# Kernel optimization log

Hardware: AMD Instinct MI355X
Metric: run time of the kernel (lower is better)

## Reference

```python
import jax, jax.numpy as jnp
import numpy as np

DIM = 768
H = 12  # num_heads -> head width W = 64 (required by internal reshapes)


def setup_inputs() -> dict:
    key = jax.random.key(0)
    ks = jax.random.split(key, 16)
    B, S = 1, 128  # V = Q = A = 128 tokens
    d = {
        "v": jax.random.normal(ks[0], (B, S, DIM), jnp.float32),
        "q": jax.random.normal(ks[1], (B, S, DIM), jnp.float32),
        "a": jax.random.normal(ks[2], (B, S, DIM), jnp.float32),
        "v_mask": jnp.ones((B, S), jnp.bool_),  # unused by the module, kept for signature parity
        "q_mask": jnp.ones((B, S), jnp.bool_),
        "a_mask": jnp.ones((B, S), jnp.bool_),
    }
    scale = 0.02
    names = ["Wv", "Wq", "Wa", "Wvo", "Wqo", "Wao"]
    for i, n in enumerate(names):
        d[n] = jax.random.normal(ks[3 + i], (DIM, DIM), jnp.float32) * scale
        d["b" + n[1:].lower()] = jnp.zeros((DIM,), jnp.float32)
    return d


def _heads(x):
    # (B, S, D) -> (B, H, S, W)
    B, S, D = x.shape
    return x.reshape(B, S, H, D // H).transpose(0, 2, 1, 3)


def reference(v, q, a, v_mask, q_mask, a_mask,
              Wv, bv, Wq, bq, Wa, ba, Wvo, bvo, Wqo, bqo, Wao, bao):
    B, Sv, D = v.shape
    Sq, Sa = q.shape[1], a.shape[1]
    W = D // H
    nv, nq, na = Sv // 8, Sq // 8, Sa // 8

    # first projections (masks are unused in the original forward)
    vp = v @ Wv + bv
    qp = q @ Wq + bq
    ap = a @ Wa + ba
    # output projections are applied to the ALREADY-projected tensors (as in source)
    vo = vp @ Wvo + bvo
    qo = qp @ Wqo + bqo
    ao = ap @ Wao + bao

    vh, qh, ah = _heads(vp), _heads(qp), _heads(ap)          # (B,H,S,W)
    voh, qoh, aoh = _heads(vo), _heads(qo), _heads(ao)

    # trilinear scores: (B,H,V,Q,A)
    att = jnp.einsum('bhvw,bhqw,bhaw->bhvqa', vh, qh, ah) / jnp.sqrt(jnp.asarray(W, vh.dtype))
    K = nv * nq * na
    # faithful to source: view(-1, H, nv*nq*na) then softmax over last axis, view back
    att = jax.nn.softmax(att.reshape(-1, H, K), axis=-1)
    att = att.reshape(-1, H, nv, nq, na)  # dropout p=0 -> identity
    B2 = att.shape[0]

    # source uses att.size(2) (= nv) for ALL three reshapes (requires V=Q=A)
    vor = voh.reshape(B2, H, nv, -1)
    qor = qoh.reshape(B2, H, nv, -1)
    aor = aoh.reshape(B2, H, nv, -1)

    v_out = jnp.einsum('bhvqa,bhvw->bvhw', att, vor).reshape(-1, DIM)
    q_out = jnp.einsum('bhvqa,bhqw->bqhw', att, qor).reshape(-1, DIM)
    a_out = jnp.einsum('bhvqa,bhaw->bahw', att, aor).reshape(-1, DIM)
    return (v_out, q_out, a_out)
```

## Files before the change

kernel.cpp:

```cpp
#include <hip/hip_runtime.h>


#define DIM   768
#define SEQ   128
#define NH    12
#define HW    64
#define PROJ_ELEMS (SEQ * DIM)
#define QOUT_OFF   98304
#define AOUT_OFF   196608

typedef short bf16x8 __attribute__((ext_vector_type(8)));
typedef short bf16x4 __attribute__((ext_vector_type(4)));
typedef float f32x4  __attribute__((ext_vector_type(4)));

__device__ __forceinline__ short f2bf(float f) {
    unsigned u = __float_as_uint(f);
    u = (u + 0x7FFFu + ((u >> 16) & 1u)) >> 16;
    return (short)u;
}

__global__ __launch_bounds__(256) void proj_mfma_kernel(
    const float* __restrict__ A0, const float* __restrict__ A1, const float* __restrict__ A2,
    const float* __restrict__ W0, const float* __restrict__ W1, const float* __restrict__ W2,
    const float* __restrict__ b0, const float* __restrict__ b1, const float* __restrict__ b2,
    float* __restrict__ C0, float* __restrict__ C1, float* __restrict__ C2)
{
    const int mat = blockIdx.y;
    const float* __restrict__ A  = (mat == 0) ? A0 : (mat == 1) ? A1 : A2;
    const float* __restrict__ Wm = (mat == 0) ? W0 : (mat == 1) ? W1 : W2;
    const float* __restrict__ bb = (mat == 0) ? b0 : (mat == 1) ? b1 : b2;
    float* __restrict__ C        = (mat == 0) ? C0 : (mat == 1) ? C1 : C2;
    const int n0 = blockIdx.x * 32;

    __shared__ short Bl[2][32][136];

    const int t    = threadIdx.x;
    const int w    = t >> 6;
    const int lane = t & 63;
    const int fm   = lane & 15;
    const int fk   = (lane >> 4) << 3;

    const int kp = (t >> 3) << 2;
    const int np = (t & 7) << 2;

    f32x4 acc[2][2];
    #pragma unroll
    for (int mt = 0; mt < 2; ++mt)
        #pragma unroll
        for (int nt = 0; nt < 2; ++nt)
            acc[mt][nt] = (f32x4){0.f, 0.f, 0.f, 0.f};

    f32x4 wr[4];
    #pragma unroll
    for (int rr = 0; rr < 4; ++rr)
        wr[rr] = *(const f32x4*)&Wm[(kp + rr) * DIM + n0 + np];

    for (int s = 0; s < 6; ++s) {
        f32x4 wn[4];
        if (s < 5) {
            #pragma unroll
            for (int rr = 0; rr < 4; ++rr)
                wn[rr] = *(const f32x4*)&Wm[((s + 1) * 128 + kp + rr) * DIM + n0 + np];
        }
        f32x4 alo[2][4], ahi[2][4];
        #pragma unroll
        for (int mt = 0; mt < 2; ++mt)
            #pragma unroll
            for (int ks = 0; ks < 4; ++ks) {
                const float* pa = &A[(32 * w + 16 * mt + fm) * DIM + s * 128 + 32 * ks + fk];
                alo[mt][ks] = *(const f32x4*)pa;
                ahi[mt][ks] = *(const f32x4*)(pa + 4);
            }
        const int buf = s & 1;
        #pragma unroll
        for (int c = 0; c < 4; ++c) {
            bf16x4 pk;
            pk[0] = f2bf(wr[0][c]); pk[1] = f2bf(wr[1][c]);
            pk[2] = f2bf(wr[2][c]); pk[3] = f2bf(wr[3][c]);
            *(bf16x4*)&Bl[buf][np + c][kp] = pk;
        }
        __syncthreads();
        #pragma unroll
        for (int ks = 0; ks < 4; ++ks) {
            bf16x8 bfr0 = *(const bf16x8*)&Bl[buf][fm     ][32 * ks + fk];
            bf16x8 bfr1 = *(const bf16x8*)&Bl[buf][16 + fm][32 * ks + fk];
            #pragma unroll
            for (int mt = 0; mt < 2; ++mt) {
                bf16x8 afr;
                afr[0] = f2bf(alo[mt][ks][0]); afr[1] = f2bf(alo[mt][ks][1]);
                afr[2] = f2bf(alo[mt][ks][2]); afr[3] = f2bf(alo[mt][ks][3]);
                afr[4] = f2bf(ahi[mt][ks][0]); afr[5] = f2bf(ahi[mt][ks][1]);
                afr[6] = f2bf(ahi[mt][ks][2]); afr[7] = f2bf(ahi[mt][ks][3]);
                acc[mt][0] = __builtin_amdgcn_mfma_f32_16x16x32_bf16(afr, bfr0, acc[mt][0], 0, 0, 0);
                acc[mt][1] = __builtin_amdgcn_mfma_f32_16x16x32_bf16(afr, bfr1, acc[mt][1], 0, 0, 0);
            }
        }
        #pragma unroll
        for (int rr = 0; rr < 4; ++rr) wr[rr] = wn[rr];
    }

    const int quad4 = (lane >> 4) << 2;
    #pragma unroll
    for (int mt = 0; mt < 2; ++mt) {
        const int row0 = 32 * w + 16 * mt + quad4;
        #pragma unroll
        for (int nt = 0; nt < 2; ++nt) {
            const int col  = n0 + 16 * nt + fm;
            const float bi = bb[col];
            #pragma unroll
            for (int rr = 0; rr < 4; ++rr)
                C[(row0 + rr) * DIM + col] = acc[mt][nt][rr] + bi;
        }
    }
}

__device__ __forceinline__ float fetch_o(const float* __restrict__ p, int idx) {
    return p[((idx >> 6) & 127) * DIM + (idx >> 13) * HW + (idx & 63)];
}

__global__ __launch_bounds__(256) void fused_attn_kernel(
    const float* __restrict__ vp, const float* __restrict__ qp, const float* __restrict__ ap,
    const float* __restrict__ vo, const float* __restrict__ qo, const float* __restrict__ ao,
    float* __restrict__ out)
{
    const int vtok = blockIdx.x;
    const int h    = blockIdx.y;

    __shared__ short vqL[128][72];
    __shared__ short ahL[128][72];

    const int t    = threadIdx.x;
    const int w    = t >> 6;
    const int lane = t & 63;
    const int fm   = lane & 15;
    const int fk   = (lane >> 4) << 3;

    {
        const int r     = t >> 1;
        const int hh    = (t & 1) << 5;
        const int gcol  = h * HW + hh;
        bf16x8 vqpk[4], ahpk[4];
        #pragma unroll
        for (int u = 0; u < 8; ++u) {
            f32x4 q4 = *(const f32x4*)&qp[r    * DIM + gcol + 4 * u];
            f32x4 v4 = *(const f32x4*)&vp[vtok * DIM + gcol + 4 * u];
            f32x4 a4 = *(const f32x4*)&ap[r    * DIM + gcol + 4 * u];
            #pragma unroll
            for (int c = 0; c < 4; ++c) {
                const int idx = 4 * u + c;
                vqpk[idx >> 3][idx & 7] = f2bf(q4[c] * v4[c]);
                ahpk[idx >> 3][idx & 7] = f2bf(a4[c]);
            }
        }
        #pragma unroll
        for (int u2 = 0; u2 < 4; ++u2) {
            *(bf16x8*)&vqL[r][hh + 8 * u2] = vqpk[u2];
            *(bf16x8*)&ahL[r][hh + 8 * u2] = ahpk[u2];
        }
    }
    __syncthreads();

    f32x4 acc[2][8];
    #pragma unroll
    for (int qt = 0; qt < 2; ++qt)
        #pragma unroll
        for (int at = 0; at < 8; ++at)
            acc[qt][at] = (f32x4){0.f, 0.f, 0.f, 0.f};

    const int q0 = 32 * w;
    #pragma unroll
    for (int ks = 0; ks < 2; ++ks) {
        bf16x8 afr0 = *(const bf16x8*)&vqL[q0 + fm     ][32 * ks + fk];
        bf16x8 afr1 = *(const bf16x8*)&vqL[q0 + 16 + fm][32 * ks + fk];
        #pragma unroll
        for (int at = 0; at < 8; ++at) {
            bf16x8 bfr = *(const bf16x8*)&ahL[16 * at + fm][32 * ks + fk];
            acc[0][at] = __builtin_amdgcn_mfma_f32_16x16x32_bf16(afr0, bfr, acc[0][at], 0, 0, 0);
            acc[1][at] = __builtin_amdgcn_mfma_f32_16x16x32_bf16(afr1, bfr, acc[1][at], 0, 0, 0);
        }
    }

    float mx = -1e30f;
    #pragma unroll
    for (int qt = 0; qt < 2; ++qt)
        #pragma unroll
        for (int at = 0; at < 8; ++at)
            #pragma unroll
            for (int rr = 0; rr < 4; ++rr) {
                acc[qt][at][rr] *= 0.125f;
                mx = fmaxf(mx, acc[qt][at][rr]);
            }
    #pragma unroll
    for (int d = 1; d < 64; d <<= 1) mx = fmaxf(mx, __shfl_xor(mx, d, 64));

    float sv[2][2] = {{0.f, 0.f}, {0.f, 0.f}};
    float sq[2][8];
    #pragma unroll
    for (int i = 0; i < 2; ++i)
        #pragma unroll
        for (int j = 0; j < 8; ++j) sq[i][j] = 0.f;
    float sa = 0.f;
    #pragma unroll
    for (int qt = 0; qt < 2; ++qt)
        #pragma unroll
        for (int at = 0; at < 8; ++at)
            #pragma unroll
            for (int rr = 0; rr < 4; ++rr) {
                const float e = __expf(acc[qt][at][rr] - mx);
                sv[qt][rr >> 1] += e;
                sq[rr & 1][at]  += e;
                sa += e;
            }
    float tot = sv[0][0] + sv[0][1] + sv[1][0] + sv[1][1];

    #pragma unroll
    for (int d = 1; d < 64; d <<= 1) tot += __shfl_xor(tot, d, 64);
    #pragma unroll
    for (int dd = 0; dd < 4; ++dd) {
        const int d = 1 << dd;
        #pragma unroll
        for (int qt = 0; qt < 2; ++qt)
            #pragma unroll
            for (int rh = 0; rh < 2; ++rh)
                sv[qt][rh] += __shfl_xor(sv[qt][rh], d, 64);
    }
    #pragma unroll
    for (int dd = 0; dd < 6; ++dd) {
        const int d = 1 << dd;
        #pragma unroll
        for (int i = 0; i < 2; ++i)
            #pragma unroll
            for (int j = 0; j < 8; ++j)
                sq[i][j] += __shfl_xor(sq[i][j], d, 64);
    }
    sa += __shfl_xor(sa, 16, 64);
    sa += __shfl_xor(sa, 32, 64);

    const int g  = h * 512 + vtok * 4 + w;
    const int b2 = g / 12;
    const int h2 = g - b2 * 12;
    const float invZ = 1.0f / tot;

    if (fm == 0) {
        const int quad = lane >> 4;
        #pragma unroll
        for (int qt = 0; qt < 2; ++qt)
            #pragma unroll
            for (int rh = 0; rh < 2; ++rh) {
                const int bin = qt * 8 + quad * 2 + rh;
                out[(b2 * 16 + bin) * 12 + h2] =
                    sv[qt][rh] * invZ * fetch_o(vo, g * 16 + bin);
            }
    }
    if (lane == 0) {
        #pragma unroll
        for (int i = 0; i < 2; ++i)
            #pragma unroll
            for (int j = 0; j < 8; ++j) {
                const int bin = i * 8 + j;
                out[QOUT_OFF + (b2 * 16 + bin) * 12 + h2] =
                    sq[i][j] * invZ * fetch_o(qo, g * 16 + bin);
            }
    }
    if (lane < 16) {
        out[AOUT_OFF + (b2 * 16 + lane) * 12 + h2] =
            sa * invZ * fetch_o(ao, g * 16 + lane);
    }
}

extern "C" void kernel_launch(void* const* d_in, const int* in_sizes, int n_in,
                              void* d_out, int out_size, void* d_ws, size_t ws_size,
                              hipStream_t stream)
{
    const float* v   = (const float*)d_in[0];
    const float* q   = (const float*)d_in[1];
    const float* a   = (const float*)d_in[2];
    const float* Wv  = (const float*)d_in[6];
    const float* bv  = (const float*)d_in[7];
    const float* Wq  = (const float*)d_in[8];
    const float* bq  = (const float*)d_in[9];
    const float* Wa  = (const float*)d_in[10];
    const float* ba  = (const float*)d_in[11];
    const float* Wvo = (const float*)d_in[12];
    const float* bvo = (const float*)d_in[13];
    const float* Wqo = (const float*)d_in[14];
    const float* bqo = (const float*)d_in[15];
    const float* Wao = (const float*)d_in[16];
    const float* bao = (const float*)d_in[17];

    float* out = (float*)d_out;
    float* ws  = (float*)d_ws;
    float* vp = ws + 0 * PROJ_ELEMS;
    float* qp = ws + 1 * PROJ_ELEMS;
    float* ap = ws + 2 * PROJ_ELEMS;
    float* vo = ws + 3 * PROJ_ELEMS;
    float* qo = ws + 4 * PROJ_ELEMS;
    float* ao = ws + 5 * PROJ_ELEMS;

    proj_mfma_kernel<<<dim3(24, 3), 256, 0, stream>>>(
        v, q, a, Wv, Wq, Wa, bv, bq, ba, vp, qp, ap);
    proj_mfma_kernel<<<dim3(24, 3), 256, 0, stream>>>(
        vp, qp, ap, Wvo, Wqo, Wao, bvo, bqo, bao, vo, qo, ao);
    fused_attn_kernel<<<dim3(SEQ, NH), 256, 0, stream>>>(
        vp, qp, ap, vo, qo, ao, out);
}
```

Before: 150.5 us.

## Switch to fp16 pre-transposed weights, drop softmax max pass, transpose-reduce shuffles

A new prep kernel converts and transposes all six weight matrices to fp16, and converts the three inputs to fp16, every call. The projection GEMM then loads MFMA fragments straight from global memory with no LDS staging, and the first projection writes fp16 outputs. The attention kernel reads the fp16 projections directly (ah goes straight from global, no LDS copy). It skips the softmax max subtraction, assuming scores are small enough not to overflow, and replaces the per-bin shuffle reductions with transpose-style reductions. This trades an extra kernel launch and fp16 range/precision risk for less conversion work, fewer shuffles and less LDS traffic.

```diff
diff --git a/kernel.cpp b/kernel.cpp
--- a/kernel.cpp
+++ b/kernel.cpp
@@ -6,97 +6,104 @@
 #define NH    12
 #define HW    64
 #define PROJ_ELEMS (SEQ * DIM)
+#define WELEMS     (DIM * DIM)
 #define QOUT_OFF   98304
 #define AOUT_OFF   196608
 
-typedef short bf16x8 __attribute__((ext_vector_type(8)));
-typedef short bf16x4 __attribute__((ext_vector_type(4)));
-typedef float f32x4  __attribute__((ext_vector_type(4)));
-
-__device__ __forceinline__ short f2bf(float f) {
-    unsigned u = __float_as_uint(f);
-    u = (u + 0x7FFFu + ((u >> 16) & 1u)) >> 16;
-    return (short)u;
-}
-
-__global__ __launch_bounds__(256) void proj_mfma_kernel(
-    const float* __restrict__ A0, const float* __restrict__ A1, const float* __restrict__ A2,
+typedef _Float16 f16x8 __attribute__((ext_vector_type(8)));
+typedef float    f32x4 __attribute__((ext_vector_type(4)));
+
+__global__ __launch_bounds__(256) void prep_kernel(
+    const float* __restrict__ v, const float* __restrict__ q, const float* __restrict__ a,
     const float* __restrict__ W0, const float* __restrict__ W1, const float* __restrict__ W2,
+    const float* __restrict__ W3, const float* __restrict__ W4, const float* __restrict__ W5,
+    _Float16* __restrict__ Wt,
+    _Float16* __restrict__ vI, _Float16* __restrict__ qI, _Float16* __restrict__ aI)
+{
+    const int z = blockIdx.z;
+    const int t = threadIdx.x;
+    if (z < 6) {
+        const float* W = (z == 0) ? W0 : (z == 1) ? W1 : (z == 2) ? W2
+                       : (z == 3) ? W3 : (z == 4) ? W4 : W5;
+        _Float16* WtM = Wt + z * WELEMS;
+        __shared__ _Float16 T[64][72];
+        const int k0 = blockIdx.x * 64;
+        const int n0 = blockIdx.y * 64;
+        const int c4 = (t & 15) * 4;
+        #pragma unroll
+        for (int p = 0; p < 4; ++p) {
+            const int r = (t >> 4) + 16 * p;
+            f32x4 wv = *(const f32x4*)&W[(k0 + r) * DIM + n0 + c4];
+            T[c4 + 0][r] = (_Float16)wv[0];
+            T[c4 + 1][r] = (_Float16)wv[1];
+            T[c4 + 2][r] = (_Float16)wv[2];
+            T[c4 + 3][r] = (_Float16)wv[3];
+        }
+        __syncthreads();
+        const int c2 = (t & 7) * 8;
+        #pragma unroll
+        for (int p = 0; p < 2; ++p) {
+            const int r = (t >> 3) + 32 * p;
+            *(f16x8*)&WtM[(n0 + r) * DIM + k0 + c2] = *(const f16x8*)&T[r][c2];
+        }
+    } else {
+        const int bid = blockIdx.x + 12 * blockIdx.y;
+        const int mat = bid / 48;
+        const int off = (bid - mat * 48) * 2048 + t * 8;
+        const float* src = (mat == 0) ? v : (mat == 1) ? q : a;
+        _Float16* dst    = (mat == 0) ? vI : (mat == 1) ? qI : aI;
+        f32x4 lo = *(const f32x4*)&src[off];
+        f32x4 hi = *(const f32x4*)&src[off + 4];
+        f16x8 o;
+        o[0] = (_Float16)lo[0]; o[1] = (_Float16)lo[1];
+        o[2] = (_Float16)lo[2]; o[3] = (_Float16)lo[3];
+        o[4] = (_Float16)hi[0]; o[5] = (_Float16)hi[1];
+        o[6] = (_Float16)hi[2]; o[7] = (_Float16)hi[3];
+        *(f16x8*)&dst[off] = o;
+    }
+}
+
+__global__ __launch_bounds__(256) void proj_kernel(
+    const _Float16* __restrict__ A0, const _Float16* __restrict__ A1, const _Float16* __restrict__ A2,
+    const _Float16* __restrict__ T0, const _Float16* __restrict__ T1, const _Float16* __restrict__ T2,
     const float* __restrict__ b0, const float* __restrict__ b1, const float* __restrict__ b2,
-    float* __restrict__ C0, float* __restrict__ C1, float* __restrict__ C2)
+    void* __restrict__ C0, void* __restrict__ C1, void* __restrict__ C2,
+    int out_f16)
 {
     const int mat = blockIdx.y;
-    const float* __restrict__ A  = (mat == 0) ? A0 : (mat == 1) ? A1 : A2;
-    const float* __restrict__ Wm = (mat == 0) ? W0 : (mat == 1) ? W1 : W2;
-    const float* __restrict__ bb = (mat == 0) ? b0 : (mat == 1) ? b1 : b2;
-    float* __restrict__ C        = (mat == 0) ? C0 : (mat == 1) ? C1 : C2;
-    const int n0 = blockIdx.x * 32;
-
-    __shared__ short Bl[2][32][136];
-
+    const _Float16* __restrict__ A = (mat == 0) ? A0 : (mat == 1) ? A1 : A2;
+    const _Float16* __restrict__ T = (mat == 0) ? T0 : (mat == 1) ? T1 : T2;
+    const float* __restrict__ bb   = (mat == 0) ? b0 : (mat == 1) ? b1 : b2;
+    void* __restrict__ C           = (mat == 0) ? C0 : (mat == 1) ? C1 : C2;
+
+    const int n0   = blockIdx.x * 32;
     const int t    = threadIdx.x;
     const int w    = t >> 6;
     const int lane = t & 63;
     const int fm   = lane & 15;
     const int fk   = (lane >> 4) << 3;
 
-    const int kp = (t >> 3) << 2;
-    const int np = (t & 7) << 2;
+    const _Float16* pa0 = A + (32 * w + fm) * DIM + fk;
+    const _Float16* pa1 = pa0 + 16 * DIM;
+    const _Float16* pb0 = T + (n0 + fm) * DIM + fk;
+    const _Float16* pb1 = pb0 + 16 * DIM;
 
     f32x4 acc[2][2];
     #pragma unroll
-    for (int mt = 0; mt < 2; ++mt)
-        #pragma unroll
-        for (int nt = 0; nt < 2; ++nt)
-            acc[mt][nt] = (f32x4){0.f, 0.f, 0.f, 0.f};
-
-    f32x4 wr[4];
-    #pragma unroll
-    for (int rr = 0; rr < 4; ++rr)
-        wr[rr] = *(const f32x4*)&Wm[(kp + rr) * DIM + n0 + np];
-
-    for (int s = 0; s < 6; ++s) {
-        f32x4 wn[4];
-        if (s < 5) {
-            #pragma unroll
-            for (int rr = 0; rr < 4; ++rr)
-                wn[rr] = *(const f32x4*)&Wm[((s + 1) * 128 + kp + rr) * DIM + n0 + np];
-        }
-        f32x4 alo[2][4], ahi[2][4];
-        #pragma unroll
-        for (int mt = 0; mt < 2; ++mt)
-            #pragma unroll
-            for (int ks = 0; ks < 4; ++ks) {
-                const float* pa = &A[(32 * w + 16 * mt + fm) * DIM + s * 128 + 32 * ks + fk];
-                alo[mt][ks] = *(const f32x4*)pa;
-                ahi[mt][ks] = *(const f32x4*)(pa + 4);
-            }
-        const int buf = s & 1;
-        #pragma unroll
-        for (int c = 0; c < 4; ++c) {
-            bf16x4 pk;
-            pk[0] = f2bf(wr[0][c]); pk[1] = f2bf(wr[1][c]);
-            pk[2] = f2bf(wr[2][c]); pk[3] = f2bf(wr[3][c]);
-            *(bf16x4*)&Bl[buf][np + c][kp] = pk;
-        }
-        __syncthreads();
-        #pragma unroll
-        for (int ks = 0; ks < 4; ++ks) {
-            bf16x8 bfr0 = *(const bf16x8*)&Bl[buf][fm     ][32 * ks + fk];
-            bf16x8 bfr1 = *(const bf16x8*)&Bl[buf][16 + fm][32 * ks + fk];
-            #pragma unroll
-            for (int mt = 0; mt < 2; ++mt) {
-                bf16x8 afr;
-                afr[0] = f2bf(alo[mt][ks][0]); afr[1] = f2bf(alo[mt][ks][1]);
-                afr[2] = f2bf(alo[mt][ks][2]); afr[3] = f2bf(alo[mt][ks][3]);
-                afr[4] = f2bf(ahi[mt][ks][0]); afr[5] = f2bf(ahi[mt][ks][1]);
-                afr[6] = f2bf(ahi[mt][ks][2]); afr[7] = f2bf(ahi[mt][ks][3]);
-                acc[mt][0] = __builtin_amdgcn_mfma_f32_16x16x32_bf16(afr, bfr0, acc[mt][0], 0, 0, 0);
-                acc[mt][1] = __builtin_amdgcn_mfma_f32_16x16x32_bf16(afr, bfr1, acc[mt][1], 0, 0, 0);
-            }
-        }
-        #pragma unroll
-        for (int rr = 0; rr < 4; ++rr) wr[rr] = wn[rr];
+    for (int i = 0; i < 2; ++i)
+        #pragma unroll
+        for (int j = 0; j < 2; ++j) acc[i][j] = (f32x4){0.f, 0.f, 0.f, 0.f};
+
+    #pragma unroll 4
+    for (int s = 0; s < 24; ++s) {
+        const f16x8 a0 = *(const f16x8*)(pa0 + 32 * s);
+        const f16x8 a1 = *(const f16x8*)(pa1 + 32 * s);
+        const f16x8 w0 = *(const f16x8*)(pb0 + 32 * s);
+        const f16x8 w1 = *(const f16x8*)(pb1 + 32 * s);
+        acc[0][0] = __builtin_amdgcn_mfma_f32_16x16x32_f16(a0, w0, acc[0][0], 0, 0, 0);
+        acc[0][1] = __builtin_amdgcn_mfma_f32_16x16x32_f16(a0, w1, acc[0][1], 0, 0, 0);
+        acc[1][0] = __builtin_amdgcn_mfma_f32_16x16x32_f16(a1, w0, acc[1][0], 0, 0, 0);
+        acc[1][1] = __builtin_amdgcn_mfma_f32_16x16x32_f16(a1, w1, acc[1][1], 0, 0, 0);
     }
 
     const int quad4 = (lane >> 4) << 2;
@@ -105,11 +112,14 @@
         const int row0 = 32 * w + 16 * mt + quad4;
         #pragma unroll
         for (int nt = 0; nt < 2; ++nt) {
-            const int col  = n0 + 16 * nt + fm;
+            const int col = n0 + 16 * nt + fm;
             const float bi = bb[col];
             #pragma unroll
-            for (int rr = 0; rr < 4; ++rr)
-                C[(row0 + rr) * DIM + col] = acc[mt][nt][rr] + bi;
+            for (int rr = 0; rr < 4; ++rr) {
+                const float val = acc[mt][nt][rr] + bi;
+                if (out_f16) ((_Float16*)C)[(row0 + rr) * DIM + col] = (_Float16)val;
+                else         ((float*)C)[(row0 + rr) * DIM + col]    = val;
+            }
         }
     }
 }
@@ -119,15 +129,15 @@
 }
 
 __global__ __launch_bounds__(256) void fused_attn_kernel(
-    const float* __restrict__ vp, const float* __restrict__ qp, const float* __restrict__ ap,
+    const _Float16* __restrict__ vpH, const _Float16* __restrict__ qpH,
+    const _Float16* __restrict__ apH,
     const float* __restrict__ vo, const float* __restrict__ qo, const float* __restrict__ ao,
     float* __restrict__ out)
 {
     const int vtok = blockIdx.x;
     const int h    = blockIdx.y;
 
-    __shared__ short vqL[128][72];
-    __shared__ short ahL[128][72];
+    __shared__ _Float16 vqL[128][72];
 
     const int t    = threadIdx.x;
     const int w    = t >> 6;
@@ -136,26 +146,15 @@
     const int fk   = (lane >> 4) << 3;
 
     {
-        const int r     = t >> 1;
-        const int hh    = (t & 1) << 5;
-        const int gcol  = h * HW + hh;
-        bf16x8 vqpk[4], ahpk[4];
-        #pragma unroll
-        for (int u = 0; u < 8; ++u) {
-            f32x4 q4 = *(const f32x4*)&qp[r    * DIM + gcol + 4 * u];
-            f32x4 v4 = *(const f32x4*)&vp[vtok * DIM + gcol + 4 * u];
-            f32x4 a4 = *(const f32x4*)&ap[r    * DIM + gcol + 4 * u];
-            #pragma unroll
-            for (int c = 0; c < 4; ++c) {
-                const int idx = 4 * u + c;
-                vqpk[idx >> 3][idx & 7] = f2bf(q4[c] * v4[c]);
-                ahpk[idx >> 3][idx & 7] = f2bf(a4[c]);
-            }
-        }
-        #pragma unroll
-        for (int u2 = 0; u2 < 4; ++u2) {
-            *(bf16x8*)&vqL[r][hh + 8 * u2] = vqpk[u2];
-            *(bf16x8*)&ahL[r][hh + 8 * u2] = ahpk[u2];
+        const int r  = t >> 1;
+        const int kh = (t & 1) << 5;
+        const _Float16* pq = qpH + r    * DIM + h * HW + kh;
+        const _Float16* pv = vpH + vtok * DIM + h * HW + kh;
+        #pragma unroll
+        for (int u = 0; u < 4; ++u) {
+            const f16x8 qv = *(const f16x8*)(pq + 8 * u);
+            const f16x8 vv = *(const f16x8*)(pv + 8 * u);
+            *(f16x8*)&vqL[r][kh + 8 * u] = qv * vv;
         }
     }
     __syncthreads();
@@ -170,99 +169,93 @@
     const int q0 = 32 * w;
     #pragma unroll
     for (int ks = 0; ks < 2; ++ks) {
-        bf16x8 afr0 = *(const bf16x8*)&vqL[q0 + fm     ][32 * ks + fk];
-        bf16x8 afr1 = *(const bf16x8*)&vqL[q0 + 16 + fm][32 * ks + fk];
+        const f16x8 af0 = *(const f16x8*)&vqL[q0 + fm     ][32 * ks + fk];
+        const f16x8 af1 = *(const f16x8*)&vqL[q0 + 16 + fm][32 * ks + fk];
         #pragma unroll
         for (int at = 0; at < 8; ++at) {
-            bf16x8 bfr = *(const bf16x8*)&ahL[16 * at + fm][32 * ks + fk];
-            acc[0][at] = __builtin_amdgcn_mfma_f32_16x16x32_bf16(afr0, bfr, acc[0][at], 0, 0, 0);
-            acc[1][at] = __builtin_amdgcn_mfma_f32_16x16x32_bf16(afr1, bfr, acc[1][at], 0, 0, 0);
-        }
-    }
-
-    float mx = -1e30f;
+            const f16x8 bf = *(const f16x8*)&apH[(16 * at + fm) * DIM + h * HW + 32 * ks + fk];
+            acc[0][at] = __builtin_amdgcn_mfma_f32_16x16x32_f16(af0, bf, acc[0][at], 0, 0, 0);
+            acc[1][at] = __builtin_amdgcn_mfma_f32_16x16x32_f16(af1, bf, acc[1][at], 0, 0, 0);
+        }
+    }
+
+    float sv[2][2] = {{0.f, 0.f}, {0.f, 0.f}};
+    float sq[2][8];
+    #pragma unroll
+    for (int i = 0; i < 2; ++i)
+        #pragma unroll
+        for (int j = 0; j < 8; ++j) sq[i][j] = 0.f;
+    float sa = 0.f;
     #pragma unroll
     for (int qt = 0; qt < 2; ++qt)
         #pragma unroll
         for (int at = 0; at < 8; ++at)
             #pragma unroll
             for (int rr = 0; rr < 4; ++rr) {
-                acc[qt][at][rr] *= 0.125f;
-                mx = fmaxf(mx, acc[qt][at][rr]);
-            }
-    #pragma unroll
-    for (int d = 1; d < 64; d <<= 1) mx = fmaxf(mx, __shfl_xor(mx, d, 64));
-
-    float sv[2][2] = {{0.f, 0.f}, {0.f, 0.f}};
-    float sq[2][8];
-    #pragma unroll
-    for (int i = 0; i < 2; ++i)
-        #pragma unroll
-        for (int j = 0; j < 8; ++j) sq[i][j] = 0.f;
-    float sa = 0.f;
-    #pragma unroll
-    for (int qt = 0; qt < 2; ++qt)
-        #pragma unroll
-        for (int at = 0; at < 8; ++at)
-            #pragma unroll
-            for (int rr = 0; rr < 4; ++rr) {
-                const float e = __expf(acc[qt][at][rr] - mx);
+                const float e = __expf(acc[qt][at][rr] * 0.125f);
                 sv[qt][rr >> 1] += e;
                 sq[rr & 1][at]  += e;
                 sa += e;
             }
-    float tot = sv[0][0] + sv[0][1] + sv[1][0] + sv[1][1];
-
-    #pragma unroll
-    for (int d = 1; d < 64; d <<= 1) tot += __shfl_xor(tot, d, 64);
-    #pragma unroll
-    for (int dd = 0; dd < 4; ++dd) {
-        const int d = 1 << dd;
-        #pragma unroll
-        for (int qt = 0; qt < 2; ++qt)
-            #pragma unroll
-            for (int rh = 0; rh < 2; ++rh)
-                sv[qt][rh] += __shfl_xor(sv[qt][rh], d, 64);
-    }
-    #pragma unroll
-    for (int dd = 0; dd < 6; ++dd) {
-        const int d = 1 << dd;
-        #pragma unroll
-        for (int i = 0; i < 2; ++i)
-            #pragma unroll
-            for (int j = 0; j < 8; ++j)
-                sq[i][j] += __shfl_xor(sq[i][j], d, 64);
-    }
-    sa += __shfl_xor(sa, 16, 64);
-    sa += __shfl_xor(sa, 32, 64);
+
+    sa += __shfl_xor(sa, 16);
+    sa += __shfl_xor(sa, 32);
+    float tot = sa;
+    tot += __shfl_xor(tot, 1);
+    tot += __shfl_xor(tot, 2);
+    tot += __shfl_xor(tot, 4);
+    tot += __shfl_xor(tot, 8);
+    const bool b0 = lane & 1;
+    const bool b1 = lane & 2;
+    float sF;
+    {
+        float snd0 = b0 ? sv[0][0] : sv[1][0];
+        float snd1 = b0 ? sv[0][1] : sv[1][1];
+        float r0 = __shfl_xor(snd0, 1);
+        float r1 = __shfl_xor(snd1, 1);
+        float s0 = (b0 ? sv[1][0] : sv[0][0]) + r0;
+        float s1 = (b0 ? sv[1][1] : sv[0][1]) + r1;
+        float snd = b1 ? s0 : s1;
+        float r2 = __shfl_xor(snd, 2);
+        sF = (b1 ? s1 : s0) + r2;
+    }
+    sF += __shfl_xor(sF, 4);
+    sF += __shfl_xor(sF, 8);
+    float s[16];
+    #pragma unroll
+    for (int i = 0; i < 2; ++i)
+        #pragma unroll
+        for (int j = 0; j < 8; ++j) s[i * 8 + j] = sq[i][j];
+    #pragma unroll
+    for (int k = 0; k < 4; ++k) {
+        const int d = 1 << k;
+        const int m = 16 >> (k + 1);
+        const bool b = (lane >> k) & 1;
+        #pragma unroll
+        for (int x = 0; x < m; ++x) {
+            const float snd = b ? s[x] : s[x + m];
+            const float rcv = __shfl_xor(snd, d);
+            s[x] = (b ? s[x + m] : s[x]) + rcv;
+        }
+    }
+    s[0] += __shfl_xor(s[0], 16);
+    s[0] += __shfl_xor(s[0], 32);
 
     const int g  = h * 512 + vtok * 4 + w;
     const int b2 = g / 12;
     const int h2 = g - b2 * 12;
     const float invZ = 1.0f / tot;
 
-    if (fm == 0) {
+    if (fm < 4) {
         const int quad = lane >> 4;
-        #pragma unroll
-        for (int qt = 0; qt < 2; ++qt)
-            #pragma unroll
-            for (int rh = 0; rh < 2; ++rh) {
-                const int bin = qt * 8 + quad * 2 + rh;
-                out[(b2 * 16 + bin) * 12 + h2] =
-                    sv[qt][rh] * invZ * fetch_o(vo, g * 16 + bin);
-            }
-    }
-    if (lane == 0) {
-        #pragma unroll
-        for (int i = 0; i < 2; ++i)
-            #pragma unroll
-            for (int j = 0; j < 8; ++j) {
-                const int bin = i * 8 + j;
-                out[QOUT_OFF + (b2 * 16 + bin) * 12 + h2] =
-                    sq[i][j] * invZ * fetch_o(qo, g * 16 + bin);
-            }
+        const int bin  = (fm & 1) * 8 + quad * 2 + ((fm >> 1) & 1);
+        out[(b2 * 16 + bin) * 12 + h2] = sF * invZ * fetch_o(vo, g * 16 + bin);
     }
     if (lane < 16) {
+        const int qbin = 8 * (lane & 1) + 4 * ((lane >> 1) & 1)
+                       + 2 * ((lane >> 2) & 1) + (lane >> 3);
+        out[QOUT_OFF + (b2 * 16 + qbin) * 12 + h2] =
+            s[0] * invZ * fetch_o(qo, g * 16 + qbin);
         out[AOUT_OFF + (b2 * 16 + lane) * 12 + h2] =
             sa * invZ * fetch_o(ao, g * 16 + lane);
     }
@@ -289,18 +282,26 @@
     const float* bao = (const float*)d_in[17];
 
     float* out = (float*)d_out;
-    float* ws  = (float*)d_ws;
-    float* vp = ws + 0 * PROJ_ELEMS;
-    float* qp = ws + 1 * PROJ_ELEMS;
-    float* ap = ws + 2 * PROJ_ELEMS;
-    float* vo = ws + 3 * PROJ_ELEMS;
-    float* qo = ws + 4 * PROJ_ELEMS;
-    float* ao = ws + 5 * PROJ_ELEMS;
-
-    proj_mfma_kernel<<<dim3(24, 3), 256, 0, stream>>>(
-        v, q, a, Wv, Wq, Wa, bv, bq, ba, vp, qp, ap);
-    proj_mfma_kernel<<<dim3(24, 3), 256, 0, stream>>>(
-        vp, qp, ap, Wvo, Wqo, Wao, bvo, bqo, bao, vo, qo, ao);
+
+    _Float16* Wt  = (_Float16*)d_ws;
+    _Float16* vI  = Wt + 6 * WELEMS;
+    _Float16* qI  = vI + PROJ_ELEMS;
+    _Float16* aI  = qI + PROJ_ELEMS;
+    _Float16* vpH = aI + PROJ_ELEMS;
+    _Float16* qpH = vpH + PROJ_ELEMS;
+    _Float16* apH = qpH + PROJ_ELEMS;
+    float*    vo  = (float*)(apH + PROJ_ELEMS);
+    float*    qo  = vo + PROJ_ELEMS;
+    float*    ao  = qo + PROJ_ELEMS;
+
+    prep_kernel<<<dim3(12, 12, 7), 256, 0, stream>>>(
+        v, q, a, Wv, Wq, Wa, Wvo, Wqo, Wao, Wt, vI, qI, aI);
+    proj_kernel<<<dim3(24, 3), 256, 0, stream>>>(
+        vI, qI, aI, Wt, Wt + WELEMS, Wt + 2 * WELEMS,
+        bv, bq, ba, vpH, qpH, apH, 1);
+    proj_kernel<<<dim3(24, 3), 256, 0, stream>>>(
+        vpH, qpH, apH, Wt + 3 * WELEMS, Wt + 4 * WELEMS, Wt + 5 * WELEMS,
+        bvo, bqo, bao, vo, qo, ao, 0);
     fused_attn_kernel<<<dim3(SEQ, NH), 256, 0, stream>>>(
-        vp, qp, ap, vo, qo, ao, out);
-}
+        vpH, qpH, apH, vo, qo, ao, out);
+}
```

Result: slower. 158.7 us (+5.5%).
